# Optimization experiments

Hardware: AMD Instinct MI355X
Metric: run time of the kernel (lower is better)

The kernel has to match this reference:

```python
import jax, jax.numpy as jnp
import numpy as np

B, S, SE, D, H, DK, DV, DH = 4, 1024, 1024, 1024, 16, 64, 64, 4096
EPS = 1e-5


def _layernorm(x, g, b):
    m = jnp.mean(x, -1, keepdims=True)
    v = jnp.mean((x - m) ** 2, -1, keepdims=True)
    return g * (x - m) / jnp.sqrt(v + EPS) + b


def _mha(q_in, k_in, v_in, mask, Wq, bq, Wk, bk, Wv, bv, Wo, bo):
    # Per-head projections fused into batched einsums (equivalent to the
    # original per-head nn.Linear loop; concat order == head order).
    Q = jnp.einsum('bsd,hdk->bhsk', q_in, Wq) + bq[None, :, None, :]
    K = jnp.einsum('bsd,hdk->bhsk', k_in, Wk) + bk[None, :, None, :]
    V = jnp.einsum('bsd,hdv->bhsv', v_in, Wv) + bv[None, :, None, :]
    scores = jnp.einsum('bhqe,bhke->bhqk', Q, K) / jnp.sqrt(jnp.float32(DK))
    scores = jnp.where(mask[:, None], jnp.float32(-1e9), scores)
    attn = jax.nn.softmax(scores, axis=-1)
    out = jnp.einsum('bhqk,bhkv->bhqv', attn, V)  # (B,H,Q,DV)
    b_, h_, q_, v_ = out.shape
    out = out.transpose(0, 2, 1, 3).reshape(b_, q_, h_ * v_)  # concat heads
    return out @ Wo + bo


def setup_inputs() -> dict:
    key = jax.random.key(0)
    ks = jax.random.split(key, 24)
    sc = 0.02
    p = lambda k, shp: (jax.random.normal(k, shp, jnp.float32) * sc)
    causal = jnp.broadcast_to(jnp.triu(jnp.ones((S, S), jnp.bool_), 1), (B, S, S))
    return {
        'input': jax.random.normal(ks[0], (B, S, D), jnp.float32),
        'input_mask': causal,
        'encoder_output': jax.random.normal(ks[1], (B, SE, D), jnp.float32),
        'enc_mask': jnp.zeros((B, S, SE), jnp.bool_),
        # masked self-attn params
        'Wq1': p(ks[2], (H, D, DK)), 'bq1': p(ks[3], (H, DK)),
        'Wk1': p(ks[4], (H, D, DK)), 'bk1': p(ks[5], (H, DK)),
        'Wv1': p(ks[6], (H, D, DV)), 'bv1': p(ks[7], (H, DV)),
        'Wo1': p(ks[8], (H * DV, D)), 'bo1': jnp.zeros((D,), jnp.float32),
        # cross-attn params
        'Wq2': p(ks[9], (H, D, DK)), 'bq2': p(ks[10], (H, DK)),
        'Wk2': p(ks[11], (H, D, DK)), 'bk2': p(ks[12], (H, DK)),
        'Wv2': p(ks[13], (H, D, DV)), 'bv2': p(ks[14], (H, DV)),
        'Wo2': p(ks[15], (H * DV, D)), 'bo2': jnp.zeros((D,), jnp.float32),
        # FFN params
        'W1f': p(ks[16], (D, DH)), 'b1f': jnp.zeros((DH,), jnp.float32),
        'W2f': p(ks[17], (DH, D)), 'b2f': jnp.zeros((D,), jnp.float32),
        # LayerNorm params
        'g1': jnp.ones((D,), jnp.float32), 'be1': jnp.zeros((D,), jnp.float32),
        'g2': jnp.ones((D,), jnp.float32), 'be2': jnp.zeros((D,), jnp.float32),
        'g3': jnp.ones((D,), jnp.float32), 'be3': jnp.zeros((D,), jnp.float32),
    }


def reference(input, input_mask, encoder_output, enc_mask,
              Wq1, bq1, Wk1, bk1, Wv1, bv1, Wo1, bo1,
              Wq2, bq2, Wk2, bk2, Wv2, bv2, Wo2, bo2,
              W1f, b1f, W2f, b2f, g1, be1, g2, be2, g3, be3):
    x = input
    out = _mha(x, x, x, input_mask, Wq1, bq1, Wk1, bk1, Wv1, bv1, Wo1, bo1)
    x1 = _layernorm(out + x, g1, be1)
    out = _mha(x1, encoder_output, encoder_output, enc_mask,
               Wq2, bq2, Wk2, bk2, Wv2, bv2, Wo2, bo2)
    x2 = _layernorm(out + x1, g2, be2)
    ffn = jax.nn.relu(x2 @ W1f + b1f) @ W2f + b2f
    return _layernorm(ffn + x2, g3, be3)
```

## Files before the change

kernel.cpp:

```cpp
#include <hip/hip_runtime.h>
#include <stdint.h>

typedef __bf16 bf16;
typedef __bf16 bf16x8 __attribute__((ext_vector_type(8)));
typedef float f32x4 __attribute__((ext_vector_type(4)));
typedef unsigned int u32;
typedef unsigned short u16;

#define DEV static __device__ __forceinline__

DEV float bf2f(u16 u){ u32 x = ((u32)u) << 16; float f; __builtin_memcpy(&f, &x, 4); return f; }

DEV float ld_f(const void* p, long i, int isb){
  return isb ? bf2f(((const u16*)p)[i]) : ((const float*)p)[i];
}

DEV void gload16(const void* g, void* l){
  __builtin_amdgcn_global_load_lds(
      (const __attribute__((address_space(1))) u32*)g,
      (__attribute__((address_space(3))) u32*)l, 16, 0, 0);
}

#define MFMA16(a,b,c) __builtin_amdgcn_mfma_f32_16x16x32_bf16(a,b,c,0,0,0)

__global__ void k_detect(const u32* in0, int* flag){
  int t = threadIdx.x;
  int cnt = 0;
  for(int i = t; i < 1024; i += 256){
    float v = bf2f((u16)(in0[i] & 0xFFFFu));
    float a = fabsf(v);
    if(a > 0.0009f && a < 16.0f) cnt++;
  }
  __shared__ int s[256];
  s[t] = cnt; __syncthreads();
  for(int o = 128; o > 0; o >>= 1){ if(t < o) s[t] += s[t+o]; __syncthreads(); }
  if(t == 0) flag[0] = (s[0] > 512) ? 1 : 0;
}

__global__ void k_cast(const void* src, bf16* dst, int n, const int* flag){
  int isb = *flag;
  int i = blockIdx.x*blockDim.x + threadIdx.x;
  int stride = gridDim.x*blockDim.x;
  for(; i < n; i += stride) dst[i] = (bf16)ld_f(src, i, isb);
}

__global__ void k_bias(const void* bq1,const void* bk1,const void* bv1,const void* bo1,
                       const void* bq2,const void* bk2,const void* bv2,const void* bo2,
                       const void* b1f,const void* b2f,
                       const void* g1,const void* be1,const void* g2,const void* be2,
                       const void* g3,const void* be3,
                       float* dst, const int* flag){
  int isb = *flag;
  int i = blockIdx.x*256 + threadIdx.x;
  if(i >= 19456) return;
  const void* s; long off;
  if(i < 3072){ if(i<1024){s=bq1;off=i;} else if(i<2048){s=bk1;off=i-1024;} else {s=bv1;off=i-2048;} }
  else if(i < 4096){s=bo1;off=i-3072;}
  else if(i < 5120){s=bq2;off=i-4096;}
  else if(i < 7168){ if(i<6144){s=bk2;off=i-5120;} else {s=bv2;off=i-6144;} }
  else if(i < 8192){s=bo2;off=i-7168;}
  else if(i < 12288){s=b1f;off=i-8192;}
  else if(i < 13312){s=b2f;off=i-12288;}
  else if(i < 14336){s=g1;off=i-13312;}
  else if(i < 15360){s=be1;off=i-14336;}
  else if(i < 16384){s=g2;off=i-15360;}
  else if(i < 17408){s=be2;off=i-16384;}
  else if(i < 18432){s=g3;off=i-17408;}
  else {s=be3;off=i-18432;}
  dst[i] = ld_f(s, off, isb);
}

__global__ void k_pack(const void* src, bf16* dst, int K_, int N_, long srcZstride,
                       int dstZrows, int row0, int Ktot, const int* flag){
  int isb = *flag;
  __shared__ float tile[64][65];
  int bx = blockIdx.x, by = blockIdx.y, z = blockIdx.z;
  long base = (long)z * srcZstride;
  int t = threadIdx.x, tr = t >> 6, tc = t & 63;
  for(int p = 0; p < 16; p++){
    int r = p*4 + tr;
    long idx = base + (long)(bx*64 + r)*N_ + by*64 + tc;
    tile[r][tc] = ld_f(src, idx, isb);
  }
  __syncthreads();
  for(int p = 0; p < 16; p++){
    int r = p*4 + tr;
    long drow = (long)row0 + (long)z*dstZrows + by*64 + r;
    dst[drow*Ktot + bx*64 + tc] = (bf16)tile[tc][r];
  }
}

__global__ void k_vtrans(const bf16* src, bf16* dst, int srcStride){
  __shared__ float tile[64][65];
  int kt = blockIdx.x, bh = blockIdx.y;
  int b = bh >> 4, h = bh & 15;
  int t = threadIdx.x, tr = t >> 6, tc = t & 63;
  const bf16* s = src + ((long)(b*1024 + kt*64))*srcStride + h*64;
  for(int p = 0; p < 16; p++){
    int r = p*4 + tr;
    tile[r][tc] = (float)s[(long)r*srcStride + tc];
  }
  __syncthreads();
  bf16* d = dst + ((long)bh*64)*1024 + kt*64;
  for(int p = 0; p < 16; p++){
    int r = p*4 + tr;
    d[(long)r*1024 + tc] = (bf16)tile[tc][r];
  }
}

template<int ACT>
__launch_bounds__(256)
__global__ void k_gemm(const bf16* __restrict__ A, const bf16* __restrict__ Bt,
                       const float* __restrict__ bias, bf16* __restrict__ C,
                       int M, int N, int K){
  alignas(16) __shared__ char As[16384];
  alignas(16) __shared__ char Bs[16384];
  const int tid = threadIdx.x;
  const int w = tid >> 6, l = tid & 63;
  const int wm = w >> 1, wn = w & 1;
  const int lg = l >> 4, lr = l & 15;
  const long m0 = (long)blockIdx.y * 128;
  const long n0 = (long)blockIdx.x * 128;

  f32x4 acc[4][4];
  for(int i = 0; i < 4; i++) for(int j = 0; j < 4; j++) acc[i][j] = 0.f;

  int r_st[4], cs_st[4];
  for(int i = 0; i < 4; i++){
    int o = i*4096 + tid*16;
    int r = o >> 7, c = (o >> 4) & 7;
    r_st[i] = r; cs_st[i] = (c ^ (r & 7)) * 8;
  }
  const int nk = K >> 6;
  for(int kt = 0; kt < nk; kt++){
    for(int i = 0; i < 4; i++){
      gload16(A + (m0 + r_st[i])*(long)K + kt*64 + cs_st[i], As + i*4096 + w*1024);
      gload16(Bt + (n0 + r_st[i])*(long)K + kt*64 + cs_st[i], Bs + i*4096 + w*1024);
    }
    __syncthreads();
    bf16x8 bfr[4][2];
    #pragma unroll
    for(int nf = 0; nf < 4; nf++){
      int row = wn*64 + nf*16 + lr;
      bfr[nf][0] = *(const bf16x8*)(Bs + row*128 + (((0+lg) ^ (row&7)) << 4));
      bfr[nf][1] = *(const bf16x8*)(Bs + row*128 + (((4+lg) ^ (row&7)) << 4));
    }
    #pragma unroll
    for(int mf = 0; mf < 4; mf++){
      int row = wm*64 + mf*16 + lr;
      bf16x8 a0 = *(const bf16x8*)(As + row*128 + (((0+lg) ^ (row&7)) << 4));
      bf16x8 a1 = *(const bf16x8*)(As + row*128 + (((4+lg) ^ (row&7)) << 4));
      #pragma unroll
      for(int nf = 0; nf < 4; nf++){
        acc[mf][nf] = MFMA16(a0, bfr[nf][0], acc[mf][nf]);
        acc[mf][nf] = MFMA16(a1, bfr[nf][1], acc[mf][nf]);
      }
    }
    __syncthreads();
  }
  for(int mf = 0; mf < 4; mf++){
    long mbase = m0 + wm*64 + mf*16 + lg*4;
    for(int nf = 0; nf < 4; nf++){
      long n = n0 + wn*64 + nf*16 + lr;
      float bv = bias[n];
      f32x4 a = acc[mf][nf];
      for(int j = 0; j < 4; j++){
        float v = a[j] + bv;
        if(ACT == 1) v = fmaxf(v, 0.f);
        C[(mbase + j)*(long)N + n] = (bf16)v;
      }
    }
  }
}

template<int CAUSAL>
__launch_bounds__(256)
__global__ void k_attn(const bf16* __restrict__ qb, int qStride,
                       const bf16* __restrict__ kb, int kStride,
                       const bf16* __restrict__ vt, bf16* __restrict__ out){
  alignas(16) __shared__ char sc[32*2048];
  int qt = blockIdx.x, bh = blockIdx.y;
  int b = bh >> 4, h = bh & 15;
  int q0 = qt * 32;
  int t = threadIdx.x, w = t >> 6, l = t & 63, lg = l >> 4, lr = l & 15;
  const int L = CAUSAL ? (q0 + 32) : 1024;
  const bf16* q  = qb + ((long)(b*1024 + q0))*qStride + h*64;
  const bf16* kp = kb + ((long)b*1024)*kStride + h*64;
  const bf16* vp = vt + (long)bh*64*1024;

  bf16x8 qa[2][2];
  #pragma unroll
  for(int mf = 0; mf < 2; mf++)
    #pragma unroll
    for(int ks = 0; ks < 2; ks++)
      qa[mf][ks] = *(const bf16x8*)(q + (long)(mf*16 + lr)*qStride + ks*32 + lg*8);

  int NT = L >> 4;
  for(int nt = w; nt < NT; nt += 4){
    f32x4 accq[2]; accq[0] = 0.f; accq[1] = 0.f;
    bf16x8 kf0 = *(const bf16x8*)(kp + (long)(nt*16 + lr)*kStride + lg*8);
    bf16x8 kf1 = *(const bf16x8*)(kp + (long)(nt*16 + lr)*kStride + 32 + lg*8);
    accq[0] = MFMA16(qa[0][0], kf0, accq[0]);
    accq[0] = MFMA16(qa[0][1], kf1, accq[0]);
    accq[1] = MFMA16(qa[1][0], kf0, accq[1]);
    accq[1] = MFMA16(qa[1][1], kf1, accq[1]);
    for(int mf = 0; mf < 2; mf++){
      for(int j = 0; j < 4; j++){
        int row = mf*16 + lg*4 + j;
        int col = nt*16 + lr;
        float v = accq[mf][j] * 0.125f;
        if(CAUSAL && col > q0 + row) v = -1e9f;
        int byte = row*2048 + (((col >> 3) ^ (row & 7)) << 4) + ((col & 7) << 1);
        *(bf16*)(sc + byte) = (bf16)v;
      }
    }
  }
  __syncthreads();
  int nch = L >> 3;
  for(int r = 0; r < 8; r++){
    int row = w*8 + r;
    int c0 = l, c1 = l + 64;
    bool h0 = c0 < nch, h1 = c1 < nch;
    bf16x8 v0, v1;
    float lmax = -1e30f;
    if(h0){ v0 = *(const bf16x8*)(sc + row*2048 + ((c0 ^ (row&7)) << 4));
            for(int j = 0; j < 8; j++) lmax = fmaxf(lmax, (float)v0[j]); }
    if(h1){ v1 = *(const bf16x8*)(sc + row*2048 + ((c1 ^ (row&7)) << 4));
            for(int j = 0; j < 8; j++) lmax = fmaxf(lmax, (float)v1[j]); }
    for(int o = 32; o > 0; o >>= 1) lmax = fmaxf(lmax, __shfl_xor(lmax, o));
    float e0[8], e1[8];
    float lsum = 0.f;
    if(h0) for(int j = 0; j < 8; j++){ e0[j] = __expf((float)v0[j] - lmax); lsum += e0[j]; }
    if(h1) for(int j = 0; j < 8; j++){ e1[j] = __expf((float)v1[j] - lmax); lsum += e1[j]; }
    for(int o = 32; o > 0; o >>= 1) lsum += __shfl_xor(lsum, o);
    float inv = 1.0f / lsum;
    if(h0){ bf16x8 p; for(int j = 0; j < 8; j++) p[j] = (bf16)(e0[j]*inv);
            *(bf16x8*)(sc + row*2048 + ((c0 ^ (row&7)) << 4)) = p; }
    if(h1){ bf16x8 p; for(int j = 0; j < 8; j++) p[j] = (bf16)(e1[j]*inv);
            *(bf16x8*)(sc + row*2048 + ((c1 ^ (row&7)) << 4)) = p; }
  }
  __syncthreads();
  int mf = w >> 1;
  int nfa = (w & 1) * 2;
  f32x4 o0, o1; o0 = 0.f; o1 = 0.f;
  int nks = L >> 5;
  for(int kk = 0; kk < nks; kk++){
    int arow = mf*16 + lr;
    int chunk = kk*4 + lg;
    bf16x8 pa  = *(const bf16x8*)(sc + arow*2048 + ((chunk ^ (arow&7)) << 4));
    bf16x8 vf0 = *(const bf16x8*)(vp + (long)(nfa*16 + lr)*1024 + kk*32 + lg*8);
    bf16x8 vf1 = *(const bf16x8*)(vp + (long)((nfa+1)*16 + lr)*1024 + kk*32 + lg*8);
    o0 = MFMA16(pa, vf0, o0);
    o1 = MFMA16(pa, vf1, o1);
  }
  bf16* ob = out + ((long)(b*1024 + q0))*1024 + h*64;
  for(int j = 0; j < 4; j++){
    int row = mf*16 + lg*4 + j;
    ob[(long)row*1024 + nfa*16 + lr]     = (bf16)o0[j];
    ob[(long)row*1024 + (nfa+1)*16 + lr] = (bf16)o1[j];
  }
}

template<int F32OUT>
__global__ void k_addln(const bf16* __restrict__ a, const bf16* __restrict__ b,
                        const float* __restrict__ g, const float* __restrict__ be,
                        void* __restrict__ outv){
  int row = blockIdx.x;
  int t = threadIdx.x;
  const bf16* ar = a + (long)row*1024;
  const bf16* br = b + (long)row*1024;
  float v[4];
  float s = 0.f;
  for(int j = 0; j < 4; j++){
    int c = t*4 + j;
    v[j] = (float)ar[c] + (float)br[c];
    s += v[j];
  }
  __shared__ float red[4], red2[4];
  for(int o = 32; o > 0; o >>= 1) s += __shfl_xor(s, o);
  int w = t >> 6, l = t & 63;
  if(l == 0) red[w] = s;
  __syncthreads();
  float mean = (red[0] + red[1] + red[2] + red[3]) * (1.0f/1024.0f);
  float qv = 0.f;
  for(int j = 0; j < 4; j++){ float d = v[j] - mean; qv += d*d; }
  for(int o = 32; o > 0; o >>= 1) qv += __shfl_xor(qv, o);
  if(l == 0) red2[w] = qv;
  __syncthreads();
  float var = (red2[0] + red2[1] + red2[2] + red2[3]) * (1.0f/1024.0f);
  float inv = rsqrtf(var + 1e-5f);
  for(int j = 0; j < 4; j++){
    int c = t*4 + j;
    float r = g[c]*(v[j] - mean)*inv + be[c];
    if(F32OUT) ((float*)outv)[(long)row*1024 + c] = r;
    else       ((bf16*)outv)[(long)row*1024 + c] = (bf16)r;
  }
}

extern "C" void kernel_launch(void* const* d_in, const int* in_sizes, int n_in,
                              void* d_out, int out_size, void* d_ws, size_t ws_size,
                              hipStream_t stream){
  char* ws = (char*)d_ws;
  const long OFF_FLAG = 0;
  const long OFF_XB   = 256;
  const long OFF_ENCB = OFF_XB   + 8388608;
  const long OFF_BIAS = OFF_ENCB + 8388608;
  const long OFF_BT1  = OFF_BIAS + 131072;
  const long OFF_BTO1 = OFF_BT1  + 6291456;
  const long OFF_BTQ2 = OFF_BTO1 + 2097152;
  const long OFF_BTKV2= OFF_BTQ2 + 2097152;
  const long OFF_BTO2 = OFF_BTKV2+ 4194304;
  const long OFF_BTW1 = OFF_BTO2 + 2097152;
  const long OFF_BTW2 = OFF_BTW1 + 8388608;
  const long OFF_R    = OFF_BTW2 + 8388608;
  const long OFF_Q2   = OFF_R    + 33554432;
  const long OFF_ATT  = OFF_Q2   + 8388608;
  const long OFF_PROJ = OFF_ATT  + 8388608;
  const long OFF_X1   = OFF_PROJ + 8388608;
  const long OFF_X2   = OFF_X1   + 8388608;

  const int* flag = (const int*)(ws + OFF_FLAG);
  float* biasr = (float*)(ws + OFF_BIAS);

  k_detect<<<1, 256, 0, stream>>>((const u32*)d_in[0], (int*)(ws + OFF_FLAG));
  k_cast<<<1024, 256, 0, stream>>>(d_in[0], (bf16*)(ws + OFF_XB),   4194304, flag);
  k_cast<<<1024, 256, 0, stream>>>(d_in[2], (bf16*)(ws + OFF_ENCB), 4194304, flag);
  k_bias<<<77, 256, 0, stream>>>(d_in[5], d_in[7], d_in[9], d_in[11],
                                 d_in[13], d_in[15], d_in[17], d_in[19],
                                 d_in[21], d_in[23],
                                 d_in[24], d_in[25], d_in[26], d_in[27], d_in[28], d_in[29],
                                 biasr, flag);
  k_pack<<<dim3(16,1,16), 256, 0, stream>>>(d_in[4],  (bf16*)(ws+OFF_BT1),  1024,   64, 65536L, 64,    0, 1024, flag);
  k_pack<<<dim3(16,1,16), 256, 0, stream>>>(d_in[6],  (bf16*)(ws+OFF_BT1),  1024,   64, 65536L, 64, 1024, 1024, flag);
  k_pack<<<dim3(16,1,16), 256, 0, stream>>>(d_in[8],  (bf16*)(ws+OFF_BT1),  1024,   64, 65536L, 64, 2048, 1024, flag);
  k_pack<<<dim3(16,16,1), 256, 0, stream>>>(d_in[10], (bf16*)(ws+OFF_BTO1), 1024, 1024, 0L,      0,    0, 1024, flag);
  k_pack<<<dim3(16,1,16), 256, 0, stream>>>(d_in[12], (bf16*)(ws+OFF_BTQ2), 1024,   64, 65536L, 64,    0, 1024, flag);
  k_pack<<<dim3(16,1,16), 256, 0, stream>>>(d_in[14], (bf16*)(ws+OFF_BTKV2),1024,   64, 65536L, 64,    0, 1024, flag);
  k_pack<<<dim3(16,1,16), 256, 0, stream>>>(d_in[16], (bf16*)(ws+OFF_BTKV2),1024,   64, 65536L, 64, 1024, 1024, flag);
  k_pack<<<dim3(16,16,1), 256, 0, stream>>>(d_in[18], (bf16*)(ws+OFF_BTO2), 1024, 1024, 0L,      0,    0, 1024, flag);
  k_pack<<<dim3(16,64,1), 256, 0, stream>>>(d_in[20], (bf16*)(ws+OFF_BTW1), 1024, 4096, 0L,      0,    0, 1024, flag);
  k_pack<<<dim3(64,16,1), 256, 0, stream>>>(d_in[22], (bf16*)(ws+OFF_BTW2), 4096, 1024, 0L,      0,    0, 4096, flag);

  k_gemm<0><<<dim3(24,32), 256, 0, stream>>>((bf16*)(ws+OFF_XB), (bf16*)(ws+OFF_BT1),
                                             biasr + 0, (bf16*)(ws+OFF_R), 4096, 3072, 1024);
  k_vtrans<<<dim3(16,64), 256, 0, stream>>>((bf16*)(ws+OFF_R) + 2048, (bf16*)(ws+OFF_R+25165824), 3072);
  k_attn<1><<<dim3(32,64), 256, 0, stream>>>((bf16*)(ws+OFF_R), 3072,
                                             (bf16*)(ws+OFF_R) + 1024, 3072,
                                             (bf16*)(ws+OFF_R+25165824), (bf16*)(ws+OFF_ATT));
  k_gemm<0><<<dim3(8,32), 256, 0, stream>>>((bf16*)(ws+OFF_ATT), (bf16*)(ws+OFF_BTO1),
                                            biasr + 3072, (bf16*)(ws+OFF_PROJ), 4096, 1024, 1024);
  k_addln<0><<<4096, 256, 0, stream>>>((bf16*)(ws+OFF_PROJ), (bf16*)(ws+OFF_XB),
                                       biasr + 13312, biasr + 14336, (void*)(ws+OFF_X1));
  k_gemm<0><<<dim3(8,32), 256, 0, stream>>>((bf16*)(ws+OFF_X1), (bf16*)(ws+OFF_BTQ2),
                                            biasr + 4096, (bf16*)(ws+OFF_Q2), 4096, 1024, 1024);
  k_gemm<0><<<dim3(16,32), 256, 0, stream>>>((bf16*)(ws+OFF_ENCB), (bf16*)(ws+OFF_BTKV2),
                                             biasr + 5120, (bf16*)(ws+OFF_R), 4096, 2048, 1024);
  k_vtrans<<<dim3(16,64), 256, 0, stream>>>((bf16*)(ws+OFF_R) + 1024, (bf16*)(ws+OFF_R+16777216), 2048);
  k_attn<0><<<dim3(32,64), 256, 0, stream>>>((bf16*)(ws+OFF_Q2), 1024,
                                             (bf16*)(ws+OFF_R), 2048,
                                             (bf16*)(ws+OFF_R+16777216), (bf16*)(ws+OFF_ATT));
  k_gemm<0><<<dim3(8,32), 256, 0, stream>>>((bf16*)(ws+OFF_ATT), (bf16*)(ws+OFF_BTO2),
                                            biasr + 7168, (bf16*)(ws+OFF_PROJ), 4096, 1024, 1024);
  k_addln<0><<<4096, 256, 0, stream>>>((bf16*)(ws+OFF_PROJ), (bf16*)(ws+OFF_X1),
                                       biasr + 15360, biasr + 16384, (void*)(ws+OFF_X2));
  k_gemm<1><<<dim3(32,32), 256, 0, stream>>>((bf16*)(ws+OFF_X2), (bf16*)(ws+OFF_BTW1),
                                             biasr + 8192, (bf16*)(ws+OFF_R), 4096, 4096, 1024);
  k_gemm<0><<<dim3(8,32), 256, 0, stream>>>((bf16*)(ws+OFF_R), (bf16*)(ws+OFF_BTW2),
                                            biasr + 12288, (bf16*)(ws+OFF_PROJ), 4096, 1024, 4096);
  k_addln<1><<<4096, 256, 0, stream>>>((bf16*)(ws+OFF_PROJ), (bf16*)(ws+OFF_X2),
                                       biasr + 17408, biasr + 18432, d_out);
}
```

Baseline: 792.4 us.

## Replace materialized-score attention with per-wave online-softmax flash attention

The attention kernel no longer writes a full 32x1024 score tile to shared memory with block-wide syncs and a separate softmax pass. Each wave now owns 16 query rows and streams 64-key tiles, keeping running max and sum in registers and rescaling the output accumulators. Only a small per-wave LDS buffer is used to re-layout probabilities for the PV MFMA. The grid is halved to 64 queries per block. This cuts LDS footprint and barriers and should raise occupancy, at the cost of extra exp and rescale work. K/V reads are not shared across waves, and the causal tail now falls on single waves, so work per wave is unbalanced.

New measurement: 795.7 us. Within noise of the previous version (+0.4%).

```diff
diff --git a/kernel.cpp b/kernel.cpp
--- a/kernel.cpp
+++ b/kernel.cpp
@@ -178,87 +178,109 @@
 __global__ void k_attn(const bf16* __restrict__ qb, int qStride,
                        const bf16* __restrict__ kb, int kStride,
                        const bf16* __restrict__ vt, bf16* __restrict__ out){
-  alignas(16) __shared__ char sc[32*2048];
-  int qt = blockIdx.x, bh = blockIdx.y;
+  alignas(16) __shared__ char pl[4*2048];
+  int bh = blockIdx.y;
   int b = bh >> 4, h = bh & 15;
-  int q0 = qt * 32;
   int t = threadIdx.x, w = t >> 6, l = t & 63, lg = l >> 4, lr = l & 15;
-  const int L = CAUSAL ? (q0 + 32) : 1024;
-  const bf16* q  = qb + ((long)(b*1024 + q0))*qStride + h*64;
+  int q0 = blockIdx.x*64 + w*16;
+  const bf16* qp = qb + ((long)(b*1024 + q0))*qStride + h*64;
   const bf16* kp = kb + ((long)b*1024)*kStride + h*64;
   const bf16* vp = vt + (long)bh*64*1024;
-
-  bf16x8 qa[2][2];
+  char* pw = pl + w*2048;
+
+  bf16x8 qa[2];
+  qa[0] = *(const bf16x8*)(qp + (long)lr*qStride + lg*8);
+  qa[1] = *(const bf16x8*)(qp + (long)lr*qStride + 32 + lg*8);
+
+  f32x4 o[4];
+  o[0] = 0.f; o[1] = 0.f; o[2] = 0.f; o[3] = 0.f;
+  float m[4]    = {-1e30f,-1e30f,-1e30f,-1e30f};
+  float lsum[4] = {0.f,0.f,0.f,0.f};
+
+  const int nkt = CAUSAL ? ((q0 >> 6) + 1) : 16;
+  for(int kt = 0; kt < nkt; kt++){
+    int kt0 = kt << 6;
+    f32x4 s4[4];
+    #pragma unroll
+    for(int tt = 0; tt < 4; tt++){
+      s4[tt] = 0.f;
+      const bf16* kr = kp + (long)(kt0 + tt*16 + lr)*kStride;
+      bf16x8 kf0 = *(const bf16x8*)(kr + lg*8);
+      bf16x8 kf1 = *(const bf16x8*)(kr + 32 + lg*8);
+      s4[tt] = MFMA16(qa[0], kf0, s4[tt]);
+      s4[tt] = MFMA16(qa[1], kf1, s4[tt]);
+    }
+    #pragma unroll
+    for(int tt = 0; tt < 4; tt++)
+      #pragma unroll
+      for(int j = 0; j < 4; j++){
+        float v = s4[tt][j] * 0.125f;
+        if(CAUSAL && kt == nkt-1){
+          int key = kt0 + tt*16 + lr;
+          int qq  = q0 + lg*4 + j;
+          if(key > qq) v = -1e9f;
+        }
+        s4[tt][j] = v;
+      }
+    float scal[4];
+    #pragma unroll
+    for(int j = 0; j < 4; j++){
+      float tmax = fmaxf(fmaxf(s4[0][j], s4[1][j]), fmaxf(s4[2][j], s4[3][j]));
+      tmax = fmaxf(tmax, __shfl_xor(tmax, 1));
+      tmax = fmaxf(tmax, __shfl_xor(tmax, 2));
+      tmax = fmaxf(tmax, __shfl_xor(tmax, 4));
+      tmax = fmaxf(tmax, __shfl_xor(tmax, 8));
+      float mnew = fmaxf(m[j], tmax);
+      float sc = __expf(m[j] - mnew);
+      m[j] = mnew;
+      float rs = 0.f;
+      #pragma unroll
+      for(int tt = 0; tt < 4; tt++){
+        float p = __expf(s4[tt][j] - mnew);
+        s4[tt][j] = p;
+        rs += p;
+      }
+      rs += __shfl_xor(rs, 1);
+      rs += __shfl_xor(rs, 2);
+      rs += __shfl_xor(rs, 4);
+      rs += __shfl_xor(rs, 8);
+      lsum[j] = lsum[j]*sc + rs;
+      scal[j] = sc;
+    }
+    #pragma unroll
+    for(int g = 0; g < 4; g++){
+      f32x4 og = o[g];
+      og[0] *= scal[0]; og[1] *= scal[1]; og[2] *= scal[2]; og[3] *= scal[3];
+      o[g] = og;
+    }
+    #pragma unroll
+    for(int tt = 0; tt < 4; tt++)
+      #pragma unroll
+      for(int j = 0; j < 4; j++){
+        int qq = lg*4 + j;
+        int byte = (qq*128 + (tt*16 + lr)*2) ^ ((qq & 7) << 4);
+        *(bf16*)(pw + byte) = (bf16)s4[tt][j];
+      }
+    bf16x8 pa0 = *(const bf16x8*)(pw + ((lr*128 +      lg*16) ^ ((lr & 7) << 4)));
+    bf16x8 pa1 = *(const bf16x8*)(pw + ((lr*128 + 64 + lg*16) ^ ((lr & 7) << 4)));
+    #pragma unroll
+    for(int g = 0; g < 4; g++){
+      const bf16* vr = vp + (long)(g*16 + lr)*1024 + kt0;
+      bf16x8 vf0 = *(const bf16x8*)(vr + lg*8);
+      bf16x8 vf1 = *(const bf16x8*)(vr + 32 + lg*8);
+      o[g] = MFMA16(pa0, vf0, o[g]);
+      o[g] = MFMA16(pa1, vf1, o[g]);
+    }
+  }
+  bf16* ob = out + ((long)(b*1024 + q0))*1024 + h*64;
+  float inv[4];
   #pragma unroll
-  for(int mf = 0; mf < 2; mf++)
-    #pragma unroll
-    for(int ks = 0; ks < 2; ks++)
-      qa[mf][ks] = *(const bf16x8*)(q + (long)(mf*16 + lr)*qStride + ks*32 + lg*8);
-
-  int NT = L >> 4;
-  for(int nt = w; nt < NT; nt += 4){
-    f32x4 accq[2]; accq[0] = 0.f; accq[1] = 0.f;
-    bf16x8 kf0 = *(const bf16x8*)(kp + (long)(nt*16 + lr)*kStride + lg*8);
-    bf16x8 kf1 = *(const bf16x8*)(kp + (long)(nt*16 + lr)*kStride + 32 + lg*8);
-    accq[0] = MFMA16(qa[0][0], kf0, accq[0]);
-    accq[0] = MFMA16(qa[0][1], kf1, accq[0]);
-    accq[1] = MFMA16(qa[1][0], kf0, accq[1]);
-    accq[1] = MFMA16(qa[1][1], kf1, accq[1]);
-    for(int mf = 0; mf < 2; mf++){
-      for(int j = 0; j < 4; j++){
-        int row = mf*16 + lg*4 + j;
-        int col = nt*16 + lr;
-        float v = accq[mf][j] * 0.125f;
-        if(CAUSAL && col > q0 + row) v = -1e9f;
-        int byte = row*2048 + (((col >> 3) ^ (row & 7)) << 4) + ((col & 7) << 1);
-        *(bf16*)(sc + byte) = (bf16)v;
-      }
-    }
-  }
-  __syncthreads();
-  int nch = L >> 3;
-  for(int r = 0; r < 8; r++){
-    int row = w*8 + r;
-    int c0 = l, c1 = l + 64;
-    bool h0 = c0 < nch, h1 = c1 < nch;
-    bf16x8 v0, v1;
-    float lmax = -1e30f;
-    if(h0){ v0 = *(const bf16x8*)(sc + row*2048 + ((c0 ^ (row&7)) << 4));
-            for(int j = 0; j < 8; j++) lmax = fmaxf(lmax, (float)v0[j]); }
-    if(h1){ v1 = *(const bf16x8*)(sc + row*2048 + ((c1 ^ (row&7)) << 4));
-            for(int j = 0; j < 8; j++) lmax = fmaxf(lmax, (float)v1[j]); }
-    for(int o = 32; o > 0; o >>= 1) lmax = fmaxf(lmax, __shfl_xor(lmax, o));
-    float e0[8], e1[8];
-    float lsum = 0.f;
-    if(h0) for(int j = 0; j < 8; j++){ e0[j] = __expf((float)v0[j] - lmax); lsum += e0[j]; }
-    if(h1) for(int j = 0; j < 8; j++){ e1[j] = __expf((float)v1[j] - lmax); lsum += e1[j]; }
-    for(int o = 32; o > 0; o >>= 1) lsum += __shfl_xor(lsum, o);
-    float inv = 1.0f / lsum;
-    if(h0){ bf16x8 p; for(int j = 0; j < 8; j++) p[j] = (bf16)(e0[j]*inv);
-            *(bf16x8*)(sc + row*2048 + ((c0 ^ (row&7)) << 4)) = p; }
-    if(h1){ bf16x8 p; for(int j = 0; j < 8; j++) p[j] = (bf16)(e1[j]*inv);
-            *(bf16x8*)(sc + row*2048 + ((c1 ^ (row&7)) << 4)) = p; }
-  }
-  __syncthreads();
-  int mf = w >> 1;
-  int nfa = (w & 1) * 2;
-  f32x4 o0, o1; o0 = 0.f; o1 = 0.f;
-  int nks = L >> 5;
-  for(int kk = 0; kk < nks; kk++){
-    int arow = mf*16 + lr;
-    int chunk = kk*4 + lg;
-    bf16x8 pa  = *(const bf16x8*)(sc + arow*2048 + ((chunk ^ (arow&7)) << 4));
-    bf16x8 vf0 = *(const bf16x8*)(vp + (long)(nfa*16 + lr)*1024 + kk*32 + lg*8);
-    bf16x8 vf1 = *(const bf16x8*)(vp + (long)((nfa+1)*16 + lr)*1024 + kk*32 + lg*8);
-    o0 = MFMA16(pa, vf0, o0);
-    o1 = MFMA16(pa, vf1, o1);
-  }
-  bf16* ob = out + ((long)(b*1024 + q0))*1024 + h*64;
-  for(int j = 0; j < 4; j++){
-    int row = mf*16 + lg*4 + j;
-    ob[(long)row*1024 + nfa*16 + lr]     = (bf16)o0[j];
-    ob[(long)row*1024 + (nfa+1)*16 + lr] = (bf16)o1[j];
-  }
+  for(int j = 0; j < 4; j++) inv[j] = 1.0f / lsum[j];
+  #pragma unroll
+  for(int g = 0; g < 4; g++)
+    #pragma unroll
+    for(int j = 0; j < 4; j++)
+      ob[(long)(lg*4 + j)*1024 + g*16 + lr] = (bf16)(o[g][j]*inv[j]);
 }
 
 template<int F32OUT>
@@ -344,7 +366,7 @@
   k_gemm<0><<<dim3(24,32), 256, 0, stream>>>((bf16*)(ws+OFF_XB), (bf16*)(ws+OFF_BT1),
                                              biasr + 0, (bf16*)(ws+OFF_R), 4096, 3072, 1024);
   k_vtrans<<<dim3(16,64), 256, 0, stream>>>((bf16*)(ws+OFF_R) + 2048, (bf16*)(ws+OFF_R+25165824), 3072);
-  k_attn<1><<<dim3(32,64), 256, 0, stream>>>((bf16*)(ws+OFF_R), 3072,
+  k_attn<1><<<dim3(16,64), 256, 0, stream>>>((bf16*)(ws+OFF_R), 3072,
                                              (bf16*)(ws+OFF_R) + 1024, 3072,
                                              (bf16*)(ws+OFF_R+25165824), (bf16*)(ws+OFF_ATT));
   k_gemm<0><<<dim3(8,32), 256, 0, stream>>>((bf16*)(ws+OFF_ATT), (bf16*)(ws+OFF_BTO1),
@@ -356,7 +378,7 @@
   k_gemm<0><<<dim3(16,32), 256, 0, stream>>>((bf16*)(ws+OFF_ENCB), (bf16*)(ws+OFF_BTKV2),
                                              biasr + 5120, (bf16*)(ws+OFF_R), 4096, 2048, 1024);
   k_vtrans<<<dim3(16,64), 256, 0, stream>>>((bf16*)(ws+OFF_R) + 1024, (bf16*)(ws+OFF_R+16777216), 2048);
-  k_attn<0><<<dim3(32,64), 256, 0, stream>>>((bf16*)(ws+OFF_Q2), 1024,
+  k_attn<0><<<dim3(16,64), 256, 0, stream>>>((bf16*)(ws+OFF_Q2), 1024,
                                              (bf16*)(ws+OFF_R), 2048,
                                              (bf16*)(ws+OFF_R+16777216), (bf16*)(ws+OFF_ATT));
   k_gemm<0><<<dim3(8,32), 256, 0, stream>>>((bf16*)(ws+OFF_ATT), (bf16*)(ws+OFF_BTO2),
```
